# Performance work log

Measured on AMD Instinct MI355X. Metric: run time of the kernel, lower is better.

The kernel has to match this reference:

```python
import jax, jax.numpy as jnp
import numpy as np

N_ATOMS = 20000
N_EDGES = 640000
ATOM_DIM = 16
BOND_DIM = 16


def setup_inputs() -> dict:
    key = jax.random.key(0)
    k1, k2, k3, k4 = jax.random.split(key, 4)
    atom_features = jax.random.normal(k1, (N_ATOMS, ATOM_DIM), dtype=jnp.float32)
    bond_features = jax.random.normal(k2, (N_EDGES, BOND_DIM), dtype=jnp.float32)
    pair_indices = jax.random.randint(k3, (N_EDGES, 2), 0, N_ATOMS, dtype=jnp.int32)
    kernel = jax.random.normal(k4, (BOND_DIM, ATOM_DIM * ATOM_DIM), dtype=jnp.float32) * 0.05
    bias = jnp.zeros((ATOM_DIM * ATOM_DIM,), dtype=jnp.float32)
    return {
        "atom_features": atom_features,
        "bond_features": bond_features,
        "pair_indices": pair_indices,
        "kernel": kernel,
        "bias": bias,
    }


def reference(atom_features, bond_features, pair_indices, kernel, bias):
    E = bond_features.shape[0]
    d = atom_features.shape[-1]
    # project bond features to per-edge [d, d] transform matrices
    bond_mats = (bond_features @ kernel + bias).reshape(E, d, d)
    # gather neighbor (source) atom features per edge
    neigh = atom_features[pair_indices[:, 1]]  # [E, d]
    # batched small matvec: [E, d, d] x [E, d] -> [E, d]
    msgs = jnp.einsum("eij,ej->ei", bond_mats, neigh)
    # scatter-sum messages to destination atoms
    aggregated = jax.ops.segment_sum(msgs, pair_indices[:, 0], num_segments=atom_features.shape[0])
    return aggregated
```

## Files before the change

kernel.cpp:

```cpp
#include <hip/hip_runtime.h>
#include <stdint.h>


constexpr int DIM       = 16;
constexpr int CAP       = 64;
constexpr int OFLOW_CAP = 65536;
constexpr int GPW       = 4;

using frag_ab = __attribute__((ext_vector_type(8))) short;
using frag_cd = __attribute__((ext_vector_type(4))) float;
union ABPack { frag_ab f; uint32_t u[4]; };

__device__ __forceinline__ uint32_t pack_bf16_2(float lo, float hi) {
    return __builtin_amdgcn_perm(__float_as_uint(hi), __float_as_uint(lo), 0x07060302u);
}

__global__ __launch_bounds__(256) void msg_mfma_kernel(
    const float* __restrict__ atom, const float* __restrict__ bond,
    const int*   __restrict__ pair, const float* __restrict__ kern,
    const float* __restrict__ bias,
    int* __restrict__ counts, int* __restrict__ oflow_cnt, int* __restrict__ oflow,
    uint16_t* __restrict__ msgs, int n_edges, int n_groups)
{
    const int wave = (int)((blockIdx.x * blockDim.x + threadIdx.x) >> 6);
    const int lane = threadIdx.x & 63;
    int g0 = wave * GPW;
    if (g0 >= n_groups) return;
    int g1 = min(g0 + GPW, n_groups);

    const int col  = lane & 15;
    const int quad = lane >> 4;
    const int hb   = quad >> 1;
    const int j0   = (quad & 1) * 8;

    frag_ab bfrag[8];
#pragma unroll
    for (int c = 0; c < 8; ++c) {
        const float* wp = kern + (2 * c + hb) * 256 + col * 16 + j0;
        float4 w0 = *(const float4*)wp;
        float4 w1 = *(const float4*)(wp + 4);
        ABPack p;
        p.u[0] = pack_bf16_2(w0.x, w0.y);
        p.u[1] = pack_bf16_2(w0.z, w0.w);
        p.u[2] = pack_bf16_2(w1.x, w1.y);
        p.u[3] = pack_bf16_2(w1.z, w1.w);
        bfrag[c] = p.f;
    }
    frag_ab bias_b;
    {
        ABPack p; p.u[0] = p.u[1] = p.u[2] = p.u[3] = 0;
        if (hb == 0) {
            const float* bp2 = bias + col * 16 + j0;
            float4 w0 = *(const float4*)bp2;
            float4 w1 = *(const float4*)(bp2 + 4);
            p.u[0] = pack_bf16_2(w0.x, w0.y);
            p.u[1] = pack_bf16_2(w0.z, w0.w);
            p.u[2] = pack_bf16_2(w1.x, w1.y);
            p.u[3] = pack_bf16_2(w1.z, w1.w);
        }
        bias_b = p.f;
    }

    for (int g = g0; g < g1; ++g) {
        const int eb = g << 4;
        const int e  = eb + col;
        const int ec = min(e, n_edges - 1);

        const int2 pr = ((const int2*)pair)[ec];

        int slot = -1;
        if (quad == 0 && e < n_edges) {
            int r = atomicAdd(&counts[pr.x], 1);
            if (r < CAP) {
                slot = pr.x * CAP + r;
            } else {
                int oi = atomicAdd(oflow_cnt, 1);
                if (oi < OFLOW_CAP) oflow[oi] = e;
            }
        }

        const float* np_ = atom + (size_t)pr.y * DIM + j0;
        float4 n0 = *(const float4*)np_;
        float4 n1 = *(const float4*)(np_ + 4);
        float nb[8] = {n0.x, n0.y, n0.z, n0.w, n1.x, n1.y, n1.z, n1.w};

        const float4* bp = (const float4*)(bond + (size_t)ec * DIM);
        float4 b0 = bp[0], b1 = bp[1], b2 = bp[2], b3 = bp[3];
        float bv[16] = {b0.x, b0.y, b0.z, b0.w, b1.x, b1.y, b1.z, b1.w,
                        b2.x, b2.y, b2.z, b2.w, b3.x, b3.y, b3.z, b3.w};

        frag_cd acc = {0.f, 0.f, 0.f, 0.f};
#pragma unroll
        for (int c = 0; c < 8; ++c) {
            const float bk = bv[2 * c + hb];
            ABPack a;
            a.u[0] = pack_bf16_2(bk * nb[0], bk * nb[1]);
            a.u[1] = pack_bf16_2(bk * nb[2], bk * nb[3]);
            a.u[2] = pack_bf16_2(bk * nb[4], bk * nb[5]);
            a.u[3] = pack_bf16_2(bk * nb[6], bk * nb[7]);
            acc = __builtin_amdgcn_mfma_f32_16x16x32_bf16(a.f, bfrag[c], acc, 0, 0, 0);
        }
        {
            ABPack a; a.u[0] = a.u[1] = a.u[2] = a.u[3] = 0;
            if (hb == 0) {
                a.u[0] = pack_bf16_2(nb[0], nb[1]);
                a.u[1] = pack_bf16_2(nb[2], nb[3]);
                a.u[2] = pack_bf16_2(nb[4], nb[5]);
                a.u[3] = pack_bf16_2(nb[6], nb[7]);
            }
            acc = __builtin_amdgcn_mfma_f32_16x16x32_bf16(a.f, bias_b, acc, 0, 0, 0);
        }

#pragma unroll
        for (int r = 0; r < 4; ++r) {
            const int m = quad * 4 + r;
            const int s = __shfl(slot, m, 64);
            if (s >= 0)
                msgs[(size_t)s * DIM + col] = (uint16_t)(__float_as_uint(acc[r]) >> 16);
        }
    }
}

__global__ __launch_bounds__(256) void reduce_kernel(
    const uint16_t* __restrict__ msgs, const int* __restrict__ counts,
    float* __restrict__ out, int n_atoms)
{
    int t = blockIdx.x * blockDim.x + threadIdx.x;
    int a = t >> 3;
    if (a >= n_atoms) return;
    int c    = t & 3;
    int half = (t >> 2) & 1;

    int cnt = min(counts[a], CAP);
    const uint32_t* base = (const uint32_t*)(msgs + (size_t)a * CAP * DIM);

    float4 acc = make_float4(0.f, 0.f, 0.f, 0.f);
    for (int j = half; j < cnt; j += 2) {
        uint2 v = *(const uint2*)(base + j * 8 + c * 2);
        acc.x += __uint_as_float(v.x << 16);
        acc.y += __uint_as_float(v.x & 0xFFFF0000u);
        acc.z += __uint_as_float(v.y << 16);
        acc.w += __uint_as_float(v.y & 0xFFFF0000u);
    }
    acc.x += __shfl_xor(acc.x, 4);
    acc.y += __shfl_xor(acc.y, 4);
    acc.z += __shfl_xor(acc.z, 4);
    acc.w += __shfl_xor(acc.w, 4);
    if (half == 0)
        ((float4*)(out + (size_t)a * DIM))[c] = acc;
}

__global__ __launch_bounds__(256) void oflow_kernel(
    const float* __restrict__ atom, const float* __restrict__ bond,
    const int*   __restrict__ pair, const float* __restrict__ kern,
    const float* __restrict__ bias,
    const int* __restrict__ oflow_cnt, const int* __restrict__ oflow,
    float* __restrict__ out, int n_edges)
{
    int n = min(*oflow_cnt, OFLOW_CAP);
    for (int i = blockIdx.x * blockDim.x + threadIdx.x; i < n;
         i += gridDim.x * blockDim.x) {
        int e   = oflow[i];
        int dst = pair[2 * e + 0];
        int src = pair[2 * e + 1];
        float neigh[DIM], bnd[DIM], acc[DIM];
        for (int q = 0; q < DIM; ++q) neigh[q] = atom[(size_t)src * DIM + q];
        for (int q = 0; q < DIM; ++q) bnd[q]   = bond[(size_t)e * DIM + q];
#pragma unroll
        for (int ii = 0; ii < DIM; ++ii) {
            float d = 0.f;
#pragma unroll
            for (int j = 0; j < DIM; ++j) d = fmaf(bias[ii * DIM + j], neigh[j], d);
            acc[ii] = d;
        }
#pragma unroll 1
        for (int k = 0; k < DIM; ++k) {
            const float bk = bnd[k];
            const float* Kr = kern + k * (DIM * DIM);
#pragma unroll
            for (int ii = 0; ii < DIM; ++ii) {
                float d = 0.f;
#pragma unroll
                for (int j = 0; j < DIM; ++j) d = fmaf(Kr[ii * DIM + j], neigh[j], d);
                acc[ii] = fmaf(bk, d, acc[ii]);
            }
        }
#pragma unroll
        for (int ii = 0; ii < DIM; ++ii) atomicAdd(&out[(size_t)dst * DIM + ii], acc[ii]);
    }
}

__global__ __launch_bounds__(256) void edge_atomic_kernel(
    const float* __restrict__ atom, const float* __restrict__ bond,
    const int*   __restrict__ pair, const float* __restrict__ kern,
    const float* __restrict__ bias, float* __restrict__ out, int n_edges)
{
    int e = blockIdx.x * blockDim.x + threadIdx.x;
    if (e >= n_edges) return;
    int dst = pair[2 * e + 0];
    int src = pair[2 * e + 1];
    float neigh[DIM], bnd[DIM], acc[DIM];
    for (int q = 0; q < DIM; ++q) neigh[q] = atom[(size_t)src * DIM + q];
    for (int q = 0; q < DIM; ++q) bnd[q]   = bond[(size_t)e * DIM + q];
#pragma unroll
    for (int i = 0; i < DIM; ++i) {
        float d = 0.f;
#pragma unroll
        for (int j = 0; j < DIM; ++j) d = fmaf(bias[i * DIM + j], neigh[j], d);
        acc[i] = d;
    }
#pragma unroll 1
    for (int k = 0; k < DIM; ++k) {
        const float bk = bnd[k];
        const float* Kr = kern + k * (DIM * DIM);
#pragma unroll
        for (int i = 0; i < DIM; ++i) {
            float d = 0.f;
#pragma unroll
            for (int j = 0; j < DIM; ++j) d = fmaf(Kr[i * DIM + j], neigh[j], d);
            acc[i] = fmaf(bk, d, acc[i]);
        }
    }
#pragma unroll
    for (int i = 0; i < DIM; ++i) atomicAdd(&out[(size_t)dst * DIM + i], acc[i]);
}

extern "C" void kernel_launch(void* const* d_in, const int* in_sizes, int n_in,
                              void* d_out, int out_size, void* d_ws, size_t ws_size,
                              hipStream_t stream)
{
    const float* atom = (const float*)d_in[0];
    const float* bond = (const float*)d_in[1];
    const int*   pair = (const int*)d_in[2];
    const float* kern = (const float*)d_in[3];
    const float* bias = (const float*)d_in[4];
    float*       out  = (float*)d_out;

    const int n_edges = in_sizes[1] / DIM;
    const int n_atoms = in_sizes[0] / DIM;

    size_t counts_off = 0;
    size_t ocnt_off   = counts_off + (size_t)n_atoms * sizeof(int);
    size_t oflow_off  = ocnt_off + sizeof(int);
    size_t msgs_off   = (oflow_off + (size_t)OFLOW_CAP * sizeof(int) + 63) & ~(size_t)63;
    size_t needed     = msgs_off + (size_t)n_atoms * CAP * DIM * sizeof(uint16_t);

    const int threads = 256;

    if (ws_size >= needed) {
        int*      counts    = (int*)((char*)d_ws + counts_off);
        int*      oflow_cnt = (int*)((char*)d_ws + ocnt_off);
        int*      oflow     = (int*)((char*)d_ws + oflow_off);
        uint16_t* msgs      = (uint16_t*)((char*)d_ws + msgs_off);

        hipMemsetAsync(counts, 0, (size_t)(n_atoms + 1) * sizeof(int), stream);

        const int n_groups = (n_edges + 15) / 16;
        const int waves    = (n_groups + GPW - 1) / GPW;
        const int mblocks  = (waves * 64 + threads - 1) / threads;
        msg_mfma_kernel<<<mblocks, threads, 0, stream>>>(
            atom, bond, pair, kern, bias, counts, oflow_cnt, oflow, msgs,
            n_edges, n_groups);

        const int rthreads = n_atoms * 8;
        reduce_kernel<<<(rthreads + threads - 1) / threads, threads, 0, stream>>>(
            msgs, counts, out, n_atoms);

        oflow_kernel<<<8, threads, 0, stream>>>(
            atom, bond, pair, kern, bias, oflow_cnt, oflow, out, n_edges);
    } else {
        hipMemsetAsync(out, 0, (size_t)out_size * sizeof(float), stream);
        edge_atomic_kernel<<<(n_edges + threads - 1) / threads, threads, 0, stream>>>(
            atom, bond, pair, kern, bias, out, n_edges);
    }
}
```

Baseline: 150.1 us.

## Transpose MFMA operands for packed message stores and pad per-atom counters

Swaps the MFMA A/B operands so each lane holds four consecutive output features of one edge. This lets the message write become one packed 8-byte store instead of four scattered 2-byte stores. Per-atom counters are padded to a 64-byte stride to spread atomic contention across cache lines, and the group loop is fully unrolled. The padding enlarges the counter memset and the counter footprint by 16x, which may hurt cache locality for the atomics.

After: 146.6 us. 2.4% less time.

```diff
diff --git a/kernel.cpp b/kernel.cpp
--- a/kernel.cpp
+++ b/kernel.cpp
@@ -2,10 +2,11 @@
 #include <stdint.h>
 
 
-constexpr int DIM       = 16;
-constexpr int CAP       = 64;
+constexpr int DIM  = 16;
+constexpr int CAP  = 64;
+constexpr int CSTR = 16;
 constexpr int OFLOW_CAP = 65536;
-constexpr int GPW       = 4;
+constexpr int GPW  = 4;
 
 using frag_ab = __attribute__((ext_vector_type(8))) short;
 using frag_cd = __attribute__((ext_vector_type(4))) float;
@@ -24,16 +25,15 @@
 {
     const int wave = (int)((blockIdx.x * blockDim.x + threadIdx.x) >> 6);
     const int lane = threadIdx.x & 63;
-    int g0 = wave * GPW;
+    const int g0 = wave * GPW;
     if (g0 >= n_groups) return;
-    int g1 = min(g0 + GPW, n_groups);
 
     const int col  = lane & 15;
     const int quad = lane >> 4;
     const int hb   = quad >> 1;
     const int j0   = (quad & 1) * 8;
 
-    frag_ab bfrag[8];
+    frag_ab wfrag[8];
 #pragma unroll
     for (int c = 0; c < 8; ++c) {
         const float* wp = kern + (2 * c + hb) * 256 + col * 16 + j0;
@@ -44,9 +44,9 @@
         p.u[1] = pack_bf16_2(w0.z, w0.w);
         p.u[2] = pack_bf16_2(w1.x, w1.y);
         p.u[3] = pack_bf16_2(w1.z, w1.w);
-        bfrag[c] = p.f;
-    }
-    frag_ab bias_b;
+        wfrag[c] = p.f;
+    }
+    frag_ab bias_a;
     {
         ABPack p; p.u[0] = p.u[1] = p.u[2] = p.u[3] = 0;
         if (hb == 0) {
@@ -58,65 +58,69 @@
             p.u[2] = pack_bf16_2(w1.x, w1.y);
             p.u[3] = pack_bf16_2(w1.z, w1.w);
         }
-        bias_b = p.f;
-    }
-
-    for (int g = g0; g < g1; ++g) {
-        const int eb = g << 4;
-        const int e  = eb + col;
-        const int ec = min(e, n_edges - 1);
-
-        const int2 pr = ((const int2*)pair)[ec];
-
-        int slot = -1;
-        if (quad == 0 && e < n_edges) {
-            int r = atomicAdd(&counts[pr.x], 1);
-            if (r < CAP) {
-                slot = pr.x * CAP + r;
-            } else {
-                int oi = atomicAdd(oflow_cnt, 1);
-                if (oi < OFLOW_CAP) oflow[oi] = e;
-            }
-        }
-
-        const float* np_ = atom + (size_t)pr.y * DIM + j0;
-        float4 n0 = *(const float4*)np_;
-        float4 n1 = *(const float4*)(np_ + 4);
-        float nb[8] = {n0.x, n0.y, n0.z, n0.w, n1.x, n1.y, n1.z, n1.w};
-
-        const float4* bp = (const float4*)(bond + (size_t)ec * DIM);
-        float4 b0 = bp[0], b1 = bp[1], b2 = bp[2], b3 = bp[3];
-        float bv[16] = {b0.x, b0.y, b0.z, b0.w, b1.x, b1.y, b1.z, b1.w,
-                        b2.x, b2.y, b2.z, b2.w, b3.x, b3.y, b3.z, b3.w};
-
-        frag_cd acc = {0.f, 0.f, 0.f, 0.f};
-#pragma unroll
-        for (int c = 0; c < 8; ++c) {
-            const float bk = bv[2 * c + hb];
-            ABPack a;
-            a.u[0] = pack_bf16_2(bk * nb[0], bk * nb[1]);
-            a.u[1] = pack_bf16_2(bk * nb[2], bk * nb[3]);
-            a.u[2] = pack_bf16_2(bk * nb[4], bk * nb[5]);
-            a.u[3] = pack_bf16_2(bk * nb[6], bk * nb[7]);
-            acc = __builtin_amdgcn_mfma_f32_16x16x32_bf16(a.f, bfrag[c], acc, 0, 0, 0);
-        }
-        {
-            ABPack a; a.u[0] = a.u[1] = a.u[2] = a.u[3] = 0;
-            if (hb == 0) {
-                a.u[0] = pack_bf16_2(nb[0], nb[1]);
-                a.u[1] = pack_bf16_2(nb[2], nb[3]);
-                a.u[2] = pack_bf16_2(nb[4], nb[5]);
-                a.u[3] = pack_bf16_2(nb[6], nb[7]);
-            }
-            acc = __builtin_amdgcn_mfma_f32_16x16x32_bf16(a.f, bias_b, acc, 0, 0, 0);
-        }
-
-#pragma unroll
-        for (int r = 0; r < 4; ++r) {
-            const int m = quad * 4 + r;
-            const int s = __shfl(slot, m, 64);
-            if (s >= 0)
-                msgs[(size_t)s * DIM + col] = (uint16_t)(__float_as_uint(acc[r]) >> 16);
+        bias_a = p.f;
+    }
+
+#pragma unroll
+    for (int u = 0; u < GPW; ++u) {
+        const int g = g0 + u;
+        if (g < n_groups) {
+            const int eb = g << 4;
+            const int e  = eb + col;
+            const int ec = min(e, n_edges - 1);
+
+            const int2 pr = ((const int2*)pair)[ec];
+
+            int slot = -1;
+            if (quad == 0 && e < n_edges) {
+                int r = atomicAdd(&counts[pr.x * CSTR], 1);
+                if (r < CAP) {
+                    slot = pr.x * CAP + r;
+                } else {
+                    int oi = atomicAdd(oflow_cnt, 1);
+                    if (oi < OFLOW_CAP) oflow[oi] = e;
+                }
+            }
+
+            const float* np_ = atom + (size_t)pr.y * DIM + j0;
+            float4 n0 = *(const float4*)np_;
+            float4 n1 = *(const float4*)(np_ + 4);
+            float nb[8] = {n0.x, n0.y, n0.z, n0.w, n1.x, n1.y, n1.z, n1.w};
+
+            const float4* bp = (const float4*)(bond + (size_t)ec * DIM);
+            float4 b0 = bp[0], b1 = bp[1], b2 = bp[2], b3 = bp[3];
+            float bv[16] = {b0.x, b0.y, b0.z, b0.w, b1.x, b1.y, b1.z, b1.w,
+                            b2.x, b2.y, b2.z, b2.w, b3.x, b3.y, b3.z, b3.w};
+
+            frag_cd acc = {0.f, 0.f, 0.f, 0.f};
+#pragma unroll
+            for (int c = 0; c < 8; ++c) {
+                const float bk = bv[2 * c + hb];
+                ABPack z;
+                z.u[0] = pack_bf16_2(bk * nb[0], bk * nb[1]);
+                z.u[1] = pack_bf16_2(bk * nb[2], bk * nb[3]);
+                z.u[2] = pack_bf16_2(bk * nb[4], bk * nb[5]);
+                z.u[3] = pack_bf16_2(bk * nb[6], bk * nb[7]);
+                acc = __builtin_amdgcn_mfma_f32_16x16x32_bf16(wfrag[c], z.f, acc, 0, 0, 0);
+            }
+            {
+                ABPack z; z.u[0] = z.u[1] = z.u[2] = z.u[3] = 0;
+                if (hb == 0) {
+                    z.u[0] = pack_bf16_2(nb[0], nb[1]);
+                    z.u[1] = pack_bf16_2(nb[2], nb[3]);
+                    z.u[2] = pack_bf16_2(nb[4], nb[5]);
+                    z.u[3] = pack_bf16_2(nb[6], nb[7]);
+                }
+                acc = __builtin_amdgcn_mfma_f32_16x16x32_bf16(bias_a, z.f, acc, 0, 0, 0);
+            }
+
+            const int s = __shfl(slot, col, 64);
+            if (s >= 0) {
+                uint2 pkd;
+                pkd.x = pack_bf16_2(acc[0], acc[1]);
+                pkd.y = pack_bf16_2(acc[2], acc[3]);
+                *(uint2*)(msgs + (size_t)s * DIM + quad * 4) = pkd;
+            }
         }
     }
 }
@@ -131,7 +135,7 @@
     int c    = t & 3;
     int half = (t >> 2) & 1;
 
-    int cnt = min(counts[a], CAP);
+    int cnt = min(counts[a * CSTR], CAP);
     const uint32_t* base = (const uint32_t*)(msgs + (size_t)a * CAP * DIM);
 
     float4 acc = make_float4(0.f, 0.f, 0.f, 0.f);
@@ -240,7 +244,7 @@
     const int n_atoms = in_sizes[0] / DIM;
 
     size_t counts_off = 0;
-    size_t ocnt_off   = counts_off + (size_t)n_atoms * sizeof(int);
+    size_t ocnt_off   = counts_off + (size_t)n_atoms * CSTR * sizeof(int);
     size_t oflow_off  = ocnt_off + sizeof(int);
     size_t msgs_off   = (oflow_off + (size_t)OFLOW_CAP * sizeof(int) + 63) & ~(size_t)63;
     size_t needed     = msgs_off + (size_t)n_atoms * CAP * DIM * sizeof(uint16_t);
@@ -253,7 +257,8 @@
         int*      oflow     = (int*)((char*)d_ws + oflow_off);
         uint16_t* msgs      = (uint16_t*)((char*)d_ws + msgs_off);
 
-        hipMemsetAsync(counts, 0, (size_t)(n_atoms + 1) * sizeof(int), stream);
+        hipMemsetAsync(counts, 0, (size_t)n_atoms * CSTR * sizeof(int) + sizeof(int),
+                       stream);
 
         const int n_groups = (n_edges + 15) / 16;
         const int waves    = (n_groups + GPW - 1) / GPW;
```
